# Optimization experiments

Hardware: AMD Instinct MI355X
Metric: run time of the kernel (lower is better)

Reference implementation:

```python
import jax, jax.numpy as jnp
import numpy as np

B, IN, H = 4096, 1024, 1024


def setup_inputs() -> dict:
    key = jax.random.key(0)
    ks = jax.random.split(key, 12)
    s = float(np.sqrt(6.0 / (IN + H)))  # xavier-uniform-like scale
    u = lambda k, shp: jax.random.uniform(k, shp, jnp.float32, -s, s)
    return {
        "x": jax.random.normal(ks[0], (B, IN), jnp.float32),
        "h_prev": jax.random.normal(ks[1], (B, H), jnp.float32),
        "c_prev": jax.random.normal(ks[2], (B, H), jnp.float32),
        "n_prev": jnp.ones((B, H), jnp.float32),
        "m_prev": jnp.zeros((B, H), jnp.float32),
        "Wi_x": u(ks[3], (H, IN)), "bi": jnp.zeros((H,), jnp.float32), "Wi_h": u(ks[4], (H, H)),
        "Wf_x": u(ks[5], (H, IN)), "bf": jnp.full((H,), 2.0, jnp.float32), "Wf_h": u(ks[6], (H, H)),
        "Wz_x": u(ks[7], (H, IN)), "bz": jnp.zeros((H,), jnp.float32), "Wz_h": u(ks[8], (H, H)),
        "Wo_x": u(ks[9], (H, IN)), "bo": jnp.zeros((H,), jnp.float32), "Wo_h": u(ks[10], (H, H)),
    }


def reference(x, h_prev, c_prev, n_prev, m_prev,
              Wi_x, bi, Wi_h, Wf_x, bf, Wf_h,
              Wz_x, bz, Wz_h, Wo_x, bo, Wo_h):
    # 8 projections (x-side with bias, h-side without), torch Linear: y = x @ W.T + b
    i_tilde = x @ Wi_x.T + bi + h_prev @ Wi_h.T
    f_aff   = x @ Wf_x.T + bf + h_prev @ Wf_h.T
    z_aff   = x @ Wz_x.T + bz + h_prev @ Wz_h.T
    o_aff   = x @ Wo_x.T + bo + h_prev @ Wo_h.T

    # forget_as_exp=False path: sigmoid forget gate, log-domain stabilizer
    log_f = jnp.log(jnp.clip(jax.nn.sigmoid(f_aff), 1e-8, None))
    m_t = jnp.maximum(log_f + m_prev, i_tilde)
    i_prime = jnp.exp(i_tilde - m_t)
    f_prime = jnp.exp(log_f + m_prev - m_t)

    z = jnp.tanh(z_aff)
    c_t = f_prime * c_prev + i_prime * z
    n_t = f_prime * n_prev + i_prime
    h_t = jax.nn.sigmoid(o_aff) * (c_t / jnp.clip(n_t, 1e-6, None))
    return h_t, c_t, n_t, m_t
```

## Files before the change

### kernel.cpp

```cpp
#include <hip/hip_runtime.h>
#include <stdint.h>


#define B_DIM 4096
#define K_DIM 2048

typedef __bf16 bf16x8 __attribute__((ext_vector_type(8)));
typedef float f32x4 __attribute__((ext_vector_type(4)));
typedef unsigned short ushort8 __attribute__((ext_vector_type(8)));

__device__ __forceinline__ unsigned short f2bf(float f) {
  unsigned u = __float_as_uint(f);
  u += 0x7fffu + ((u >> 16) & 1u);
  return (unsigned short)(u >> 16);
}
__device__ __forceinline__ float bf2f(unsigned short u) {
  return __uint_as_float(((unsigned)u) << 16);
}

__device__ __forceinline__ ushort8 load8_as_bf16(const void* base, size_t off, bool isbf) {
  if (isbf) return *(const ushort8*)((const unsigned short*)base + off);
  const float* f = (const float*)base + off;
  float4 v0 = ((const float4*)f)[0];
  float4 v1 = ((const float4*)f)[1];
  ushort8 o;
  o[0] = f2bf(v0.x); o[1] = f2bf(v0.y); o[2] = f2bf(v0.z); o[3] = f2bf(v0.w);
  o[4] = f2bf(v1.x); o[5] = f2bf(v1.y); o[6] = f2bf(v1.z); o[7] = f2bf(v1.w);
  return o;
}

__global__ void pack_all(const void* __restrict__ xv, const void* __restrict__ hv,
                         const void* __restrict__ Wix, const void* __restrict__ Wih,
                         const void* __restrict__ Wfx, const void* __restrict__ Wfh,
                         const void* __restrict__ Wzx, const void* __restrict__ Wzh,
                         const void* __restrict__ Wox, const void* __restrict__ Woh,
                         unsigned short* __restrict__ Apk, unsigned short* __restrict__ Bpk) {
  const int blk = blockIdx.x;
  const int lane = threadIdx.x & 63;
  const bool isA = blk < 4096;
  const unsigned* disc = (const unsigned*)(isA ? xv : Wix);
  int v = 0;
  if (lane < 32) {
    unsigned e = (disc[lane] >> 7) & 0xFFu;
    v = (e > (isA ? 129u : 122u)) ? 1 : 0;
  }
  const bool isbf = (__ballot(v) == 0ull);

  const int k = threadIdx.x * 8;
  if (isA) {
    const int m = blk;
    const void* src = (k < 1024) ? xv : hv;
    size_t off = (size_t)m * 1024 + (k & 1023);
    *(ushort8*)(Apk + (size_t)m * 2048 + k) = load8_as_bf16(src, off, isbf);
  } else {
    const int br = blk - 4096;
    const int g = (br >> 4) & 3;
    const int wrow = ((br >> 6) << 4) | (br & 15);
    const void* W;
    if (k < 1024) W = (g == 0) ? Wix : (g == 1) ? Wfx : (g == 2) ? Wzx : Wox;
    else          W = (g == 0) ? Wih : (g == 1) ? Wfh : (g == 2) ? Wzh : Woh;
    size_t off = (size_t)wrow * 1024 + (k & 1023);
    *(ushort8*)(Bpk + (size_t)br * 2048 + k) = load8_as_bf16(W, off, isbf);
  }
}


__device__ __forceinline__ void gload16(const void* g, void* l) {
  __builtin_amdgcn_global_load_lds(
      (__attribute__((address_space(1))) void*)g,
      (__attribute__((address_space(3))) void*)l, 16, 0, 0);
}

#define SCHED0 __builtin_amdgcn_sched_barrier(0)
#define BAR    __builtin_amdgcn_s_barrier()
#define VM6    asm volatile("s_waitcnt vmcnt(6)" ::: "memory")
#define VM0    asm volatile("s_waitcnt vmcnt(0)" ::: "memory")
#define LGKM(N) asm volatile("s_waitcnt lgkmcnt(" #N ")" ::: "memory")
#define NOWAIT ((void)0)
#define NOSTAGE ((void)0)

#define STAGE_HALF(buf, ab, hf, kt) {                                          \
    _Pragma("unroll")                                                          \
    for (int r_ = 0; r_ < 2; ++r_) {                                           \
      const unsigned short* g_ = (ab ? sB : sA) +                              \
          (size_t)((r_ * 128 + (hf) * (ab ? 32 : 64)) * 2048 + (kt) * 64);     \
      gload16(g_, &lds[buf][ab][(hf) * 128 + r_ * 64 + w * 8][0]);             \
    } }

#define LDSA(buf, mh, mi, CS) \
  (*(const bf16x8*)(&lds[buf][0][0][0] + ((mh)*128 + (mi)*16)*64 + aBase + CS))
#define LDSB(buf, nh, nf, CS) \
  (*(const bf16x8*)(&lds[buf][1][0][0] + ((nh)*128 + (nf)*16)*64 + bBase + CS))

#define RD16(buf) {                                                            \
    fA[0][0]=LDSA(buf,0,0,csw0); fA[1][0]=LDSA(buf,0,1,csw0);                  \
    fA[2][0]=LDSA(buf,0,2,csw0); fA[3][0]=LDSA(buf,0,3,csw0);                  \
    fB0[0][0]=LDSB(buf,0,0,csw0); fB0[1][0]=LDSB(buf,0,1,csw0);                \
    SCHED0;                                                                    \
    fA[0][1]=LDSA(buf,0,0,csw1); fA[1][1]=LDSA(buf,0,1,csw1);                  \
    fA[2][1]=LDSA(buf,0,2,csw1); fA[3][1]=LDSA(buf,0,3,csw1);                  \
    fB0[0][1]=LDSB(buf,0,0,csw1); fB0[1][1]=LDSB(buf,0,1,csw1);                \
    SCHED0;                                                                    \
    fB1[0][0]=LDSB(buf,1,0,csw0); fB1[1][0]=LDSB(buf,1,1,csw0);                \
    fB1[0][1]=LDSB(buf,1,0,csw1); fB1[1][1]=LDSB(buf,1,1,csw1);                \
  }

#define MFMA_H(FB, MH, NH, KS) {                                               \
    __builtin_amdgcn_s_setprio(1);                                             \
    _Pragma("unroll") for (int mi = 0; mi < 4; ++mi)                           \
      _Pragma("unroll") for (int nf = 0; nf < 2; ++nf)                         \
        acc[(MH)*4+mi][(NH)*2+nf] = __builtin_amdgcn_mfma_f32_16x16x32_bf16(   \
            fA[mi][KS], FB[nf][KS], acc[(MH)*4+mi][(NH)*2+nf], 0, 0, 0);       \
    __builtin_amdgcn_s_setprio(0); }

#define MFMA_Q2(FB, MH, NH) {                                                  \
    __builtin_amdgcn_s_setprio(1);                                             \
    _Pragma("unroll") for (int mi = 0; mi < 4; ++mi)                           \
      _Pragma("unroll") for (int nf = 0; nf < 2; ++nf)                         \
        _Pragma("unroll") for (int ks = 0; ks < 2; ++ks)                       \
          acc[(MH)*4+mi][(NH)*2+nf] = __builtin_amdgcn_mfma_f32_16x16x32_bf16( \
              fA[mi][ks], FB[nf][ks], acc[(MH)*4+mi][(NH)*2+nf], 0, 0, 0);     \
    __builtin_amdgcn_s_setprio(0); }

#define PHASE1(buf, STG) {                                                     \
    RD16(buf); SCHED0; STG; SCHED0; BAR;                                       \
    LGKM(10); SCHED0;                                                          \
    MFMA_H(fB0, 0, 0, 0); SCHED0;                                              \
    LGKM(4); SCHED0;                                                           \
    MFMA_H(fB0, 0, 0, 1); SCHED0;                                              \
    BAR; SCHED0; }

#define PHASE2(buf, STG) {                                                     \
    STG; SCHED0; BAR;                                                          \
    LGKM(0); SCHED0;                                                           \
    __builtin_amdgcn_s_setprio(1);                                             \
    _Pragma("unroll") for (int mi = 0; mi < 4; ++mi) {                         \
      _Pragma("unroll") for (int nf = 0; nf < 2; ++nf)                         \
        _Pragma("unroll") for (int ks = 0; ks < 2; ++ks)                       \
          acc[mi][2+nf] = __builtin_amdgcn_mfma_f32_16x16x32_bf16(             \
              fA[mi][ks], fB1[nf][ks], acc[mi][2+nf], 0, 0, 0);                \
      fA[mi][0] = LDSA(buf, 1, mi, csw0);                                      \
      fA[mi][1] = LDSA(buf, 1, mi, csw1);                                      \
    }                                                                          \
    __builtin_amdgcn_s_setprio(0); SCHED0;                                     \
    BAR; SCHED0; }

#define PHASE3(STG) {                                                          \
    STG; SCHED0; BAR;                                                          \
    LGKM(0); SCHED0;                                                           \
    MFMA_Q2(fB1, 1, 1); SCHED0;                                                \
    BAR; SCHED0; }

#define PHASE4(STG, VMW) {                                                     \
    STG; SCHED0; BAR;                                                          \
    LGKM(0); SCHED0;                                                           \
    MFMA_Q2(fB0, 1, 0); VMW; SCHED0;                                           \
    BAR; SCHED0; }

__global__ __launch_bounds__(512, 2) void gemm_fused(
    const unsigned short* __restrict__ Apk,
    const unsigned short* __restrict__ Bpk,
    const void* __restrict__ bi, const void* __restrict__ bfg,
    const void* __restrict__ bz, const void* __restrict__ bo,
    const void* __restrict__ c_prev, const void* __restrict__ n_prev,
    const void* __restrict__ m_prev,
    float* __restrict__ out)
{
  __shared__ unsigned short lds[2][2][256][64];

  const int tid  = threadIdx.x;
  const int w    = tid >> 6;
  const int lane = tid & 63;
  const int wm   = w >> 2;
  const int wn   = w & 3;
  const int lcol = lane & 15;
  const int qrow = lane >> 4;

  const int bid = blockIdx.x;
  const int swz = (bid & 7) * 32 + (bid >> 3);
  const int bm = swz >> 4;
  const int bn = swz & 15;

  const int l3 = lane >> 3;
  const int cg = (lane & 7) ^ l3;
  const unsigned short* sA = Apk + (size_t)(bm * 256 + w * 8 + l3) * 2048 + cg * 8;
  const unsigned short* sB = Bpk + (size_t)(bn * 256 + (w >> 2) * 64 + (w & 3) * 8 + l3) * 2048 + cg * 8;

  const int csw0 = (((lane >> 4)    ) ^ (lane & 7)) * 8;
  const int csw1 = ((4 + (lane >> 4)) ^ (lane & 7)) * 8;
  const int aBase = (wm * 64 + lcol) * 64;
  const int bBase = (wn * 32 + lcol) * 64;

  f32x4 acc[8][4] = {};
  bf16x8 fA[4][2], fB0[2][2], fB1[2][2];

  STAGE_HALF(0, 0, 0, 0); SCHED0;
  STAGE_HALF(0, 1, 0, 0); SCHED0;
  STAGE_HALF(0, 1, 1, 0); SCHED0;
  STAGE_HALF(0, 0, 1, 0); SCHED0;
  STAGE_HALF(1, 0, 0, 1); SCHED0;
  STAGE_HALF(1, 1, 0, 1); SCHED0;
  STAGE_HALF(1, 1, 1, 1); SCHED0;
  VM6; SCHED0; BAR; SCHED0;

  for (int t = 0; t < 30; t += 2) {
    PHASE1(0, STAGE_HALF(1, 0, 1, t + 1));
    PHASE2(0, STAGE_HALF(0, 0, 0, t + 2));
    PHASE3(   STAGE_HALF(0, 1, 0, t + 2));
    PHASE4(   STAGE_HALF(0, 1, 1, t + 2), VM6);
    PHASE1(1, STAGE_HALF(0, 0, 1, t + 2));
    PHASE2(1, STAGE_HALF(1, 0, 0, t + 3));
    PHASE3(   STAGE_HALF(1, 1, 0, t + 3));
    PHASE4(   STAGE_HALF(1, 1, 1, t + 3), VM6);
  }
  PHASE1(0, STAGE_HALF(1, 0, 1, 31));
  PHASE2(0, NOSTAGE);
  PHASE3(   NOSTAGE);
  PHASE4(   NOSTAGE, VM0);
  PHASE1(1, NOSTAGE);
  PHASE2(1, NOSTAGE);
  PHASE3(   NOSTAGE);
  PHASE4(   NOSTAGE, NOWAIT);

  const bool sbf = (((const unsigned*)n_prev)[0] == 0x3F803F80u);
  const bool bbf = (((const unsigned*)bfg)[0]    == 0x40004000u);
  const int bcol = wn * 16 + lcol;
  const int n = bn * 64 + bcol;
  const float bi_n = bbf ? bf2f(((const unsigned short*)bi)[n])  : ((const float*)bi)[n];
  const float bf_n = bbf ? bf2f(((const unsigned short*)bfg)[n]) : ((const float*)bfg)[n];
  const float bz_n = bbf ? bf2f(((const unsigned short*)bz)[n])  : ((const float*)bz)[n];
  const float bo_n = bbf ? bf2f(((const unsigned short*)bo)[n])  : ((const float*)bo)[n];

#define GATE_MATH                                                              \
      float sf = 1.f / (1.f + __expf(-fa));                                    \
      sf = fmaxf(sf, 1e-8f);                                                   \
      float lf_ = __logf(sf);                                                  \
      float mt = fmaxf(lf_ + mp, it);                                          \
      float ip = __expf(it - mt);                                              \
      float fp = __expf(lf_ + mp - mt);                                        \
      float zc = fminf(fmaxf(za, -15.f), 15.f);                                \
      float e2 = __expf(2.f * zc);                                             \
      float z  = (e2 - 1.f) / (e2 + 1.f);                                      \
      float ct = fp * cp + ip * z;                                             \
      float nt = fp * npv + ip;                                                \
      float so = 1.f / (1.f + __expf(-oa));                                    \
      float ht = so * (ct / fmaxf(nt, 1e-6f));

  if (!sbf) {
    float* lf = (float*)&lds[0][0][0][0];
    const float* srcC = (const float*)c_prev;
    const float* srcN = (const float*)n_prev;
    const float* srcM = (const float*)m_prev;

#pragma unroll
    for (int hh = 0; hh < 2; ++hh) {
#pragma unroll
      for (int s = 0; s < 3; ++s) {
        const float* srcp = (s == 0) ? srcC : (s == 1) ? srcN : srcM;
#pragma unroll
        for (int jj = 0; jj < 4; ++jj) {
          const int j = w * 4 + jj;
          const int lr = j * 4 + qrow;
          const int grow = bm * 256 + (lr >> 6) * 128 + hh * 64 + (lr & 63);
          const float* g = srcp + (size_t)grow * 1024 + bn * 64 + lcol * 4;
          gload16(g, lf + s * 8192 + j * 256);
        }
      }
      SCHED0; VM0; SCHED0; BAR; SCHED0;

      float gc[16], gn[16], gm[16];
#pragma unroll
      for (int ml = 0; ml < 4; ++ml)
#pragma unroll
        for (int r = 0; r < 4; ++r) {
          const int off = (wm * 64 + ml * 16 + qrow * 4 + r) * 64 + bcol;
          gc[ml * 4 + r] = lf[off];
          gn[ml * 4 + r] = lf[8192 + off];
          gm[ml * 4 + r] = lf[16384 + off];
        }
      SCHED0; LGKM(0); SCHED0; BAR; SCHED0;

#pragma unroll
      for (int ml = 0; ml < 4; ++ml) {
        const int mi = hh * 4 + ml;
#pragma unroll
        for (int r = 0; r < 4; ++r) {
          const int e = ml * 4 + r;
          float it = acc[mi][0][r] + bi_n;
          float fa = acc[mi][1][r] + bf_n;
          float za = acc[mi][2][r] + bz_n;
          float oa = acc[mi][3][r] + bo_n;
          float cp = gc[e], npv = gn[e], mp = gm[e];
          GATE_MATH
          const int off = (wm * 64 + ml * 16 + qrow * 4 + r) * 64 + bcol;
          lf[off]         = ht;
          lf[8192  + off] = ct;
          lf[16384 + off] = nt;
          lf[24576 + off] = mt;
        }
      }
      SCHED0; LGKM(0); SCHED0; BAR; SCHED0;

#pragma unroll
      for (int k = 0; k < 16; ++k) {
        const int c = k * 512 + tid;
        const int s = c >> 11;
        const int cs = c & 2047;
        const int lr = cs >> 4, c4 = cs & 15;
        f32x4 v = *(const f32x4*)(lf + s * 8192 + lr * 64 + c4 * 4);
        const int grow = bm * 256 + (lr >> 6) * 128 + hh * 64 + (lr & 63);
        *(f32x4*)(out + (size_t)s * 4194304 + (size_t)grow * 1024 + bn * 64 + c4 * 4) = v;
      }
      SCHED0; LGKM(0); SCHED0; BAR; SCHED0;
    }
  } else {
    const int row0 = bm * 256 + wm * 128 + qrow * 4;
    float* out_h = out;
    float* out_c = out + 4194304;
    float* out_n = out + 2 * 4194304;
    float* out_m = out + 3 * 4194304;
#pragma unroll
    for (int mi = 0; mi < 8; ++mi) {
#pragma unroll
      for (int r = 0; r < 4; ++r) {
        const int row = row0 + mi * 16 + r;
        const size_t idx = (size_t)row * 1024 + n;
        float it = acc[mi][0][r] + bi_n;
        float fa = acc[mi][1][r] + bf_n;
        float za = acc[mi][2][r] + bz_n;
        float oa = acc[mi][3][r] + bo_n;
        float cp  = bf2f(((const unsigned short*)c_prev)[idx]);
        float npv = bf2f(((const unsigned short*)n_prev)[idx]);
        float mp  = bf2f(((const unsigned short*)m_prev)[idx]);
        GATE_MATH
        out_h[idx] = ht;
        out_c[idx] = ct;
        out_n[idx] = nt;
        out_m[idx] = mt;
      }
    }
  }
#undef GATE_MATH
}

extern "C" void kernel_launch(void* const* d_in, const int* in_sizes, int n_in,
                              void* d_out, int out_size, void* d_ws, size_t ws_size,
                              hipStream_t stream) {
  const void* x      = d_in[0];
  const void* h_prev = d_in[1];
  const void* c_prev = d_in[2];
  const void* n_prev = d_in[3];
  const void* m_prev = d_in[4];
  const void* Wi_x = d_in[5];
  const void* bi   = d_in[6];
  const void* Wi_h = d_in[7];
  const void* Wf_x = d_in[8];
  const void* bf   = d_in[9];
  const void* Wf_h = d_in[10];
  const void* Wz_x = d_in[11];
  const void* bz   = d_in[12];
  const void* Wz_h = d_in[13];
  const void* Wo_x = d_in[14];
  const void* bo   = d_in[15];
  const void* Wo_h = d_in[16];

  unsigned short* Apk = (unsigned short*)d_ws;
  unsigned short* Bpk = Apk + (size_t)B_DIM * K_DIM;

  pack_all<<<8192, 256, 0, stream>>>(x, h_prev, Wi_x, Wi_h, Wf_x, Wf_h,
                                     Wz_x, Wz_h, Wo_x, Wo_h, Apk, Bpk);
  gemm_fused<<<256, 512, 0, stream>>>(Apk, Bpk, bi, bf, bz, bo,
                                      c_prev, n_prev, m_prev,
                                      (float*)d_out);
}
```

Measured before the change: 249.9 us.

## Restructure GEMM main loop into one-barrier quadrant phases with cross-phase LDS prefetch

Replaces the four-phase main loop, which used two barriers per phase and a bulk fragment read at the start of each k-tile, with four quadrant phases that each have a single barrier. LDS fragment reads for the next buffer are interleaved into the last quadrant's MFMAs, and fB1 loads move into the first quadrant. The global staging order is rebalanced, and the prologue now issues all eight half-tiles before preloading fragments. The aim is fewer barriers and better overlap of LDS reads with MFMA. The cost is a more delicate ordering of waits and buffer reuse.

```diff
diff --git a/kernel.cpp b/kernel.cpp
--- a/kernel.cpp
+++ b/kernel.cpp
@@ -78,6 +78,7 @@
 #define LGKM(N) asm volatile("s_waitcnt lgkmcnt(" #N ")" ::: "memory")
 #define NOWAIT ((void)0)
 #define NOSTAGE ((void)0)
+#define MFMA16(a, b, c) __builtin_amdgcn_mfma_f32_16x16x32_bf16(a, b, c, 0, 0, 0)
 
 #define STAGE_HALF(buf, ab, hf, kt) {                                          \
     _Pragma("unroll")                                                          \
@@ -92,70 +93,63 @@
 #define LDSB(buf, nh, nf, CS) \
   (*(const bf16x8*)(&lds[buf][1][0][0] + ((nh)*128 + (nf)*16)*64 + bBase + CS))
 
-#define RD16(buf) {                                                            \
-    fA[0][0]=LDSA(buf,0,0,csw0); fA[1][0]=LDSA(buf,0,1,csw0);                  \
-    fA[2][0]=LDSA(buf,0,2,csw0); fA[3][0]=LDSA(buf,0,3,csw0);                  \
-    fB0[0][0]=LDSB(buf,0,0,csw0); fB0[1][0]=LDSB(buf,0,1,csw0);                \
-    SCHED0;                                                                    \
-    fA[0][1]=LDSA(buf,0,0,csw1); fA[1][1]=LDSA(buf,0,1,csw1);                  \
-    fA[2][1]=LDSA(buf,0,2,csw1); fA[3][1]=LDSA(buf,0,3,csw1);                  \
-    fB0[0][1]=LDSB(buf,0,0,csw1); fB0[1][1]=LDSB(buf,0,1,csw1);                \
-    SCHED0;                                                                    \
-    fB1[0][0]=LDSB(buf,1,0,csw0); fB1[1][0]=LDSB(buf,1,1,csw0);                \
-    fB1[0][1]=LDSB(buf,1,0,csw1); fB1[1][1]=LDSB(buf,1,1,csw1);                \
-  }
-
-#define MFMA_H(FB, MH, NH, KS) {                                               \
-    __builtin_amdgcn_s_setprio(1);                                             \
-    _Pragma("unroll") for (int mi = 0; mi < 4; ++mi)                           \
-      _Pragma("unroll") for (int nf = 0; nf < 2; ++nf)                         \
-        acc[(MH)*4+mi][(NH)*2+nf] = __builtin_amdgcn_mfma_f32_16x16x32_bf16(   \
-            fA[mi][KS], FB[nf][KS], acc[(MH)*4+mi][(NH)*2+nf], 0, 0, 0);       \
-    __builtin_amdgcn_s_setprio(0); }
-
-#define MFMA_Q2(FB, MH, NH) {                                                  \
+#define PH_Q00(buf, STG) {                                                     \
+    LGKM(0); SCHED0; BAR; SCHED0;                                              \
+    STG;                                                                       \
+    fB1[0][0] = LDSB(buf, 1, 0, csw0); fB1[1][0] = LDSB(buf, 1, 1, csw0);      \
+    fB1[0][1] = LDSB(buf, 1, 0, csw1); fB1[1][1] = LDSB(buf, 1, 1, csw1);      \
     __builtin_amdgcn_s_setprio(1);                                             \
     _Pragma("unroll") for (int mi = 0; mi < 4; ++mi)                           \
       _Pragma("unroll") for (int nf = 0; nf < 2; ++nf)                         \
         _Pragma("unroll") for (int ks = 0; ks < 2; ++ks)                       \
-          acc[(MH)*4+mi][(NH)*2+nf] = __builtin_amdgcn_mfma_f32_16x16x32_bf16( \
-              fA[mi][ks], FB[nf][ks], acc[(MH)*4+mi][(NH)*2+nf], 0, 0, 0);     \
-    __builtin_amdgcn_s_setprio(0); }
-
-#define PHASE1(buf, STG) {                                                     \
-    RD16(buf); SCHED0; STG; SCHED0; BAR;                                       \
-    LGKM(10); SCHED0;                                                          \
-    MFMA_H(fB0, 0, 0, 0); SCHED0;                                              \
-    LGKM(4); SCHED0;                                                           \
-    MFMA_H(fB0, 0, 0, 1); SCHED0;                                              \
-    BAR; SCHED0; }
-
-#define PHASE2(buf, STG) {                                                     \
-    STG; SCHED0; BAR;                                                          \
-    LGKM(0); SCHED0;                                                           \
+          acc[mi][nf] = MFMA16(fA[mi][ks], fB0[nf][ks], acc[mi][nf]);          \
+    __builtin_amdgcn_s_setprio(0);                                             \
+  }
+
+#define PH_Q01(buf, STG) {                                                     \
+    LGKM(0); SCHED0; BAR; SCHED0;                                              \
+    STG;                                                                       \
     __builtin_amdgcn_s_setprio(1);                                             \
     _Pragma("unroll") for (int mi = 0; mi < 4; ++mi) {                         \
       _Pragma("unroll") for (int nf = 0; nf < 2; ++nf)                         \
         _Pragma("unroll") for (int ks = 0; ks < 2; ++ks)                       \
-          acc[mi][2+nf] = __builtin_amdgcn_mfma_f32_16x16x32_bf16(             \
-              fA[mi][ks], fB1[nf][ks], acc[mi][2+nf], 0, 0, 0);                \
+          acc[mi][2+nf] = MFMA16(fA[mi][ks], fB1[nf][ks], acc[mi][2+nf]);      \
       fA[mi][0] = LDSA(buf, 1, mi, csw0);                                      \
       fA[mi][1] = LDSA(buf, 1, mi, csw1);                                      \
     }                                                                          \
-    __builtin_amdgcn_s_setprio(0); SCHED0;                                     \
-    BAR; SCHED0; }
-
-#define PHASE3(STG) {                                                          \
-    STG; SCHED0; BAR;                                                          \
-    LGKM(0); SCHED0;                                                           \
-    MFMA_Q2(fB1, 1, 1); SCHED0;                                                \
-    BAR; SCHED0; }
-
-#define PHASE4(STG, VMW) {                                                     \
-    STG; SCHED0; BAR;                                                          \
-    LGKM(0); SCHED0;                                                           \
-    MFMA_Q2(fB0, 1, 0); VMW; SCHED0;                                           \
-    BAR; SCHED0; }
+    __builtin_amdgcn_s_setprio(0);                                             \
+  }
+
+#define PH_Q11(STG) {                                                          \
+    LGKM(0); SCHED0; BAR; SCHED0;                                              \
+    STG;                                                                       \
+    __builtin_amdgcn_s_setprio(1);                                             \
+    _Pragma("unroll") for (int mi = 0; mi < 4; ++mi)                           \
+      _Pragma("unroll") for (int nf = 0; nf < 2; ++nf)                         \
+        _Pragma("unroll") for (int ks = 0; ks < 2; ++ks)                       \
+          acc[4+mi][2+nf] = MFMA16(fA[mi][ks], fB1[nf][ks], acc[4+mi][2+nf]);  \
+    __builtin_amdgcn_s_setprio(0);                                             \
+  }
+
+#define PH_Q10(nbuf, STG, VMW, RF) {                                           \
+    VMW; SCHED0; BAR; SCHED0;                                                  \
+    STG;                                                                       \
+    __builtin_amdgcn_s_setprio(1);                                             \
+    _Pragma("unroll") for (int mi = 0; mi < 4; ++mi)                           \
+      _Pragma("unroll") for (int ks = 0; ks < 2; ++ks)                         \
+        acc[4+mi][0] = MFMA16(fA[mi][ks], fB0[0][ks], acc[4+mi][0]);           \
+    if (RF) { fB0[0][0] = LDSB(nbuf, 0, 0, csw0);                              \
+              fB0[0][1] = LDSB(nbuf, 0, 0, csw1); }                            \
+    _Pragma("unroll") for (int mi = 0; mi < 4; ++mi) {                         \
+      _Pragma("unroll") for (int ks = 0; ks < 2; ++ks)                         \
+        acc[4+mi][1] = MFMA16(fA[mi][ks], fB0[1][ks], acc[4+mi][1]);           \
+      if (RF) { fA[mi][0] = LDSA(nbuf, 0, mi, csw0);                           \
+                fA[mi][1] = LDSA(nbuf, 0, mi, csw1); }                         \
+    }                                                                          \
+    if (RF) { fB0[1][0] = LDSB(nbuf, 0, 1, csw0);                              \
+              fB0[1][1] = LDSB(nbuf, 0, 1, csw1); }                            \
+    __builtin_amdgcn_s_setprio(0);                                             \
+  }
 
 __global__ __launch_bounds__(512, 2) void gemm_fused(
     const unsigned short* __restrict__ Apk,
@@ -201,26 +195,35 @@
   STAGE_HALF(1, 0, 0, 1); SCHED0;
   STAGE_HALF(1, 1, 0, 1); SCHED0;
   STAGE_HALF(1, 1, 1, 1); SCHED0;
-  VM6; SCHED0; BAR; SCHED0;
-
-  for (int t = 0; t < 30; t += 2) {
-    PHASE1(0, STAGE_HALF(1, 0, 1, t + 1));
-    PHASE2(0, STAGE_HALF(0, 0, 0, t + 2));
-    PHASE3(   STAGE_HALF(0, 1, 0, t + 2));
-    PHASE4(   STAGE_HALF(0, 1, 1, t + 2), VM6);
-    PHASE1(1, STAGE_HALF(0, 0, 1, t + 2));
-    PHASE2(1, STAGE_HALF(1, 0, 0, t + 3));
-    PHASE3(   STAGE_HALF(1, 1, 0, t + 3));
-    PHASE4(   STAGE_HALF(1, 1, 1, t + 3), VM6);
-  }
-  PHASE1(0, STAGE_HALF(1, 0, 1, 31));
-  PHASE2(0, NOSTAGE);
-  PHASE3(   NOSTAGE);
-  PHASE4(   NOSTAGE, VM0);
-  PHASE1(1, NOSTAGE);
-  PHASE2(1, NOSTAGE);
-  PHASE3(   NOSTAGE);
-  PHASE4(   NOSTAGE, NOWAIT);
+  STAGE_HALF(1, 0, 1, 1); SCHED0;
+  asm volatile("s_waitcnt vmcnt(8)" ::: "memory"); SCHED0; BAR; SCHED0;
+#pragma unroll
+  for (int mi = 0; mi < 4; ++mi) {
+    fA[mi][0] = LDSA(0, 0, mi, csw0);
+    fA[mi][1] = LDSA(0, 0, mi, csw1);
+  }
+  fB0[0][0] = LDSB(0, 0, 0, csw0); fB0[0][1] = LDSB(0, 0, 0, csw1);
+  fB0[1][0] = LDSB(0, 0, 1, csw0); fB0[1][1] = LDSB(0, 0, 1, csw1);
+
+  for (int i = 0; i < 15; ++i) {
+    const int tE = 2 * i + 2, tO = 2 * i + 3;
+    PH_Q00(0, STAGE_HALF(0, 0, 0, tE));
+    PH_Q01(0, STAGE_HALF(0, 1, 1, tE));
+    PH_Q11(   STAGE_HALF(0, 0, 1, tE));
+    PH_Q10(1, STAGE_HALF(0, 1, 0, tE), VM6, 1);
+    PH_Q00(1, STAGE_HALF(1, 0, 0, tO));
+    PH_Q01(1, STAGE_HALF(1, 1, 1, tO));
+    PH_Q11(   STAGE_HALF(1, 0, 1, tO));
+    PH_Q10(0, STAGE_HALF(1, 1, 0, tO), VM6, 1);
+  }
+  PH_Q00(0, NOSTAGE);
+  PH_Q01(0, NOSTAGE);
+  PH_Q11(   NOSTAGE);
+  PH_Q10(1, NOSTAGE, VM0, 1);
+  PH_Q00(1, NOSTAGE);
+  PH_Q01(1, NOSTAGE);
+  PH_Q11(   NOSTAGE);
+  PH_Q10(0, NOSTAGE, NOWAIT, 0);
 
   const bool sbf = (((const unsigned*)n_prev)[0] == 0x3F803F80u);
   const bool bbf = (((const unsigned*)bfg)[0]    == 0x40004000u);
```

Measured after the change: 253.9 us. Within noise of the previous version (+1.6%).
